# Kernel tuning notes

Hardware: AMD Instinct MI355X
Metric: run time of the kernel (lower is better)

The kernel has to match this reference:

```python
import jax, jax.numpy as jnp
import numpy as np

S_LEN, BATCH, HID, HEADS = 2048, 4, 1024, 16
HD = HID // HEADS


def setup_inputs() -> dict:
    key = jax.random.key(0)
    ks = jax.random.split(key, 6)

    def lin_w(k, out_dim, in_dim):
        return jax.random.normal(k, (out_dim, in_dim), jnp.float32) * (1.0 / np.sqrt(in_dim))

    return {
        "hidden_states": jax.random.normal(ks[0], (S_LEN, BATCH, HID), jnp.float32),
        "Wq": lin_w(ks[1], HID, HID), "bq": jnp.zeros((HID,), jnp.float32),
        "Wk": lin_w(ks[2], HID, HID), "bk": jnp.zeros((HID,), jnp.float32),
        "Wv": lin_w(ks[3], HID, HID), "bv": jnp.zeros((HID,), jnp.float32),
        "Wf": lin_w(ks[4], HEADS, HID), "bf": jnp.zeros((HEADS,), jnp.float32),
        "Wo": lin_w(ks[5], HID, HID), "bo": jnp.zeros((HID,), jnp.float32),
    }


def _forget_attention(hidden_states, Wq, bq, Wk, bk, Wv, bv, Wf, bf, Wo, bo):
    S, B, H = hidden_states.shape
    nh, hd = HEADS, HD

    def shape(x):
        return x.reshape(S, B, nh, hd)

    q = shape(hidden_states @ Wq.T + bq)
    k = shape(hidden_states @ Wk.T + bk)
    v = shape(hidden_states @ Wv.T + bv)

    # kernel_fn = elu(x) + 1
    phi_q = jax.nn.elu(q) + 1.0
    phi_k = jax.nn.elu(k) + 1.0

    f = jax.nn.sigmoid(hidden_states @ Wf.T + bf)  # [S, B, nh]

    # F_{t,j} = prod_{i=j+1}^{t} f_i  factorizes into the recurrence:
    #   S_t = f_t * S_{t-1} + phi_k_t (x) v_t ;  z_t = f_t * z_{t-1} + phi_k_t
    # out_t = (phi_q_t . S_t) / (phi_q_t . z_t + eps)
    def step(carry, xs):
        Sm, z = carry                      # [B,nh,hd,hd], [B,nh,hd]
        ft, pk, pq, vt = xs                # [B,nh], [B,nh,hd] x3
        fte = ft[..., None]
        Sm = fte[..., None] * Sm + pk[..., :, None] * vt[..., None, :]
        z = fte * z + pk
        num = jnp.einsum('bhd,bhde->bhe', pq, Sm)
        den = jnp.einsum('bhd,bhd->bh', pq, z)[..., None]
        return (Sm, z), num / (den + 1e-6)

    init = (jnp.zeros((B, nh, hd, hd), hidden_states.dtype),
            jnp.zeros((B, nh, hd), hidden_states.dtype))
    _, out = jax.lax.scan(step, init, (f, phi_k, phi_q, v))

    out = out.reshape(S, B, H) @ Wo.T + bo
    return out, f


def reference(hidden_states, Wq, bq, Wk, bk, Wv, bv, Wf, bf, Wo, bo):
    out, f = _forget_attention(hidden_states, Wq, bq, Wk, bk, Wv, bv, Wf, bf, Wo, bo)
    return (out, jnp.zeros_like(out), f)
```

## Files before the change

kernel.cpp:

```cpp
#include <hip/hip_runtime.h>
#include <hip/hip_bf16.h>
#include <math.h>

#define S_LEN 2048
#define BATCH 4
#define HID   1024
#define HEADS 16
#define HD    64
#define SB    (S_LEN*BATCH)
#define CHUNK 64
#define NCHUNK (S_LEN/CHUNK)
#define BH    (BATCH*HEADS)
#define NSTK  3200

typedef __bf16 bf16x8 __attribute__((ext_vector_type(8)));
typedef float  f32x4  __attribute__((ext_vector_type(4)));
typedef unsigned short ushort_t;
typedef unsigned short u16x8 __attribute__((ext_vector_type(8)));

__device__ __forceinline__ unsigned short f2bf(float x) {
    union { float f; unsigned int u; } un; un.f = x;
    unsigned int u = un.u;
    unsigned int r = (u + 0x7FFFu + ((u >> 16) & 1u)) >> 16;
    return (unsigned short)r;
}
__device__ __forceinline__ float bf2f(unsigned short s) {
    union { unsigned int u; float f; } un; un.u = ((unsigned int)s) << 16;
    return un.f;
}

#define NXU (SB*HID/4)
#define NW1 (NSTK*HID/4)
#define NW2 (HID*HID/4)
#define NBU (NSTK/4)
#define NTOT (NXU+NW1+NW2+NBU)

__global__ __launch_bounds__(256) void prep_kernel(
    const float* __restrict__ X,  const float* __restrict__ Wq,
    const float* __restrict__ Wk, const float* __restrict__ Wv,
    const float* __restrict__ Wf, const float* __restrict__ Wo,
    const float* __restrict__ bq, const float* __restrict__ bk,
    const float* __restrict__ bv, const float* __restrict__ bf,
    ushort_t* __restrict__ Xb, ushort_t* __restrict__ Wstk,
    ushort_t* __restrict__ Wob, float* __restrict__ bstk)
{
    const int i = blockIdx.x * 256 + threadIdx.x;
    if (i < NXU) {
        float4 v = ((const float4*)X)[i];
        ushort4 o; o.x=f2bf(v.x); o.y=f2bf(v.y); o.z=f2bf(v.z); o.w=f2bf(v.w);
        ((ushort4*)Xb)[i] = o;
    } else if (i < NXU + NW1) {
        const int idx4 = (i - NXU) * 4;
        const int row = idx4 >> 10, col = idx4 & 1023;
        float4 v;
        if      (row < 1024) v = *(const float4*)(Wq + (size_t)row*HID + col);
        else if (row < 2048) v = *(const float4*)(Wk + (size_t)(row-1024)*HID + col);
        else if (row < 3072) v = *(const float4*)(Wv + (size_t)(row-2048)*HID + col);
        else if (row < 3088) v = *(const float4*)(Wf + (size_t)(row-3072)*HID + col);
        else                 v = make_float4(0.f,0.f,0.f,0.f);
        ushort4 o; o.x=f2bf(v.x); o.y=f2bf(v.y); o.z=f2bf(v.z); o.w=f2bf(v.w);
        *(ushort4*)(Wstk + idx4) = o;
    } else if (i < NXU + NW1 + NW2) {
        const int idx4 = (i - NXU - NW1) * 4;
        float4 v = *(const float4*)(Wo + idx4);
        ushort4 o; o.x=f2bf(v.x); o.y=f2bf(v.y); o.z=f2bf(v.z); o.w=f2bf(v.w);
        *(ushort4*)(Wob + idx4) = o;
    } else if (i < NTOT) {
        const int idx4 = (i - NXU - NW1 - NW2) * 4;
        #pragma unroll
        for (int t = 0; t < 4; ++t) {
            const int c = idx4 + t;
            float v;
            if      (c < 1024) v = bq[c];
            else if (c < 2048) v = bk[c-1024];
            else if (c < 3072) v = bv[c-2048];
            else if (c < 3088) v = bf[c-3072];
            else               v = 0.f;
            bstk[c] = v;
        }
    }
}

__global__ __launch_bounds__(256) void qkvf_gemm(
    const ushort_t* __restrict__ X, const ushort_t* __restrict__ W,
    const float* __restrict__ bias,
    ushort_t* __restrict__ Q, ushort_t* __restrict__ Kr,
    ushort_t* __restrict__ KT, ushort_t* __restrict__ VT,
    float* __restrict__ f_out, float* __restrict__ logf_out)
{
    __shared__ ushort_t As[128 * 32];
    __shared__ ushort_t Bs[128 * 32];

    const int tid  = threadIdx.x;
    const int wave = tid >> 6, lane = tid & 63;
    const int waveM = wave >> 1, waveN = wave & 1;
    const int rowBase = blockIdx.y * 128;
    const int colBase = blockIdx.x * 128;
    const int K = HID;

    f32x4 acc[4][4];
    #pragma unroll
    for (int i = 0; i < 4; ++i)
        #pragma unroll
        for (int j = 0; j < 4; ++j)
            acc[i][j] = (f32x4){0.f, 0.f, 0.f, 0.f};

    const int srow = lane >> 2;
    const int scol = (lane & 3) * 8;

    const ushort_t* gA0 = X + (size_t)(rowBase + wave*16 + srow) * K + scol;
    const ushort_t* gB0 = W + (size_t)(colBase + wave*16 + srow) * K + scol;
    ushort_t* lA = As + (wave*16)*32;
    ushort_t* lB = Bs + (wave*16)*32;

    const int fr = lane & 15;
    const int fk = (lane >> 4) * 8;

    for (int k0 = 0; k0 < K; k0 += 32) {
        __builtin_amdgcn_global_load_lds(
            (const __attribute__((address_space(1))) void*)(gA0 + k0),
            (__attribute__((address_space(3))) void*)lA, 16, 0, 0);
        __builtin_amdgcn_global_load_lds(
            (const __attribute__((address_space(1))) void*)(gA0 + (size_t)64*K + k0),
            (__attribute__((address_space(3))) void*)(lA + 64*32), 16, 0, 0);
        __builtin_amdgcn_global_load_lds(
            (const __attribute__((address_space(1))) void*)(gB0 + k0),
            (__attribute__((address_space(3))) void*)lB, 16, 0, 0);
        __builtin_amdgcn_global_load_lds(
            (const __attribute__((address_space(1))) void*)(gB0 + (size_t)64*K + k0),
            (__attribute__((address_space(3))) void*)(lB + 64*32), 16, 0, 0);

        __syncthreads();

        bf16x8 a[4], b[4];
        #pragma unroll
        for (int i = 0; i < 4; ++i)
            a[i] = *(const bf16x8*)(As + (waveM*64 + i*16 + fr)*32 + fk);
        #pragma unroll
        for (int j = 0; j < 4; ++j)
            b[j] = *(const bf16x8*)(Bs + (waveN*64 + j*16 + fr)*32 + fk);

        #pragma unroll
        for (int i = 0; i < 4; ++i)
            #pragma unroll
            for (int j = 0; j < 4; ++j)
                acc[i][j] = __builtin_amdgcn_mfma_f32_16x16x32_bf16(
                    a[i], b[j], acc[i][j], 0, 0, 0);

        __syncthreads();
    }

    const int er = (lane >> 4) * 4;
    const int ec = lane & 15;
    #pragma unroll
    for (int i = 0; i < 4; ++i) {
        #pragma unroll
        for (int j = 0; j < 4; ++j) {
            const int r0 = rowBase + waveM*64 + i*16 + er;
            const int c0 = colBase + waveN*64 + j*16;
            if (c0 >= 3088) continue;
            const int c  = c0 + ec;
            const float bv = bias[c];
            #pragma unroll
            for (int k = 0; k < 4; ++k) {
                float v = acc[i][j][k] + bv;
                const int r = r0 + k;
                const int s = r >> 2, bb = r & 3;
                if (c0 < 1024) {
                    v = (v > 0.f) ? (v + 1.f) : __expf(v);
                    Q[(size_t)r * HID + c] = f2bf(v);
                } else if (c0 < 2048) {
                    v = (v > 0.f) ? (v + 1.f) : __expf(v);
                    const int cc = c - 1024;
                    const ushort_t h = f2bf(v);
                    Kr[(size_t)r * HID + cc] = h;
                    KT[(size_t)bb * ((size_t)HID*S_LEN) + (size_t)cc * S_LEN + s] = h;
                } else if (c0 < 3072) {
                    const int cc = c - 2048;
                    VT[(size_t)bb * ((size_t)HID*S_LEN) + (size_t)cc * S_LEN + s] = f2bf(v);
                } else {
                    const int n = c - 3072;
                    const float fv = 1.f / (1.f + __expf(-v));
                    f_out[(size_t)r * HEADS + n]    = fv;
                    logf_out[(size_t)r * HEADS + n] = -__logf(1.f + __expf(-v));
                }
            }
        }
    }
}

__global__ __launch_bounds__(256) void gemm_out(
    const ushort_t* __restrict__ X, const ushort_t* __restrict__ W,
    const float* __restrict__ bias, float* __restrict__ Y,
    float* __restrict__ Yzero)
{
    __shared__ ushort_t As[128 * 32];
    __shared__ ushort_t Bs[128 * 32];

    const int tid  = threadIdx.x;
    const int wave = tid >> 6, lane = tid & 63;
    const int waveM = wave >> 1, waveN = wave & 1;
    const int rowBase = blockIdx.y * 128;
    const int colBase = blockIdx.x * 128;
    const int K = HID, N = HID;

    f32x4 acc[4][4];
    #pragma unroll
    for (int i = 0; i < 4; ++i)
        #pragma unroll
        for (int j = 0; j < 4; ++j)
            acc[i][j] = (f32x4){0.f, 0.f, 0.f, 0.f};

    const int srow = lane >> 2;
    const int scol = (lane & 3) * 8;

    const ushort_t* gA0 = X + (size_t)(rowBase + wave*16 + srow) * K + scol;
    const ushort_t* gB0 = W + (size_t)(colBase + wave*16 + srow) * K + scol;
    ushort_t* lA = As + (wave*16)*32;
    ushort_t* lB = Bs + (wave*16)*32;

    const int fr = lane & 15;
    const int fk = (lane >> 4) * 8;

    for (int k0 = 0; k0 < K; k0 += 32) {
        __builtin_amdgcn_global_load_lds(
            (const __attribute__((address_space(1))) void*)(gA0 + k0),
            (__attribute__((address_space(3))) void*)lA, 16, 0, 0);
        __builtin_amdgcn_global_load_lds(
            (const __attribute__((address_space(1))) void*)(gA0 + (size_t)64*K + k0),
            (__attribute__((address_space(3))) void*)(lA + 64*32), 16, 0, 0);
        __builtin_amdgcn_global_load_lds(
            (const __attribute__((address_space(1))) void*)(gB0 + k0),
            (__attribute__((address_space(3))) void*)lB, 16, 0, 0);
        __builtin_amdgcn_global_load_lds(
            (const __attribute__((address_space(1))) void*)(gB0 + (size_t)64*K + k0),
            (__attribute__((address_space(3))) void*)(lB + 64*32), 16, 0, 0);

        __syncthreads();

        bf16x8 a[4], b[4];
        #pragma unroll
        for (int i = 0; i < 4; ++i)
            a[i] = *(const bf16x8*)(As + (waveM*64 + i*16 + fr)*32 + fk);
        #pragma unroll
        for (int j = 0; j < 4; ++j)
            b[j] = *(const bf16x8*)(Bs + (waveN*64 + j*16 + fr)*32 + fk);

        #pragma unroll
        for (int i = 0; i < 4; ++i)
            #pragma unroll
            for (int j = 0; j < 4; ++j)
                acc[i][j] = __builtin_amdgcn_mfma_f32_16x16x32_bf16(
                    a[i], b[j], acc[i][j], 0, 0, 0);

        __syncthreads();
    }

    const int er = (lane >> 4) * 4;
    const int ec = lane & 15;
    #pragma unroll
    for (int i = 0; i < 4; ++i) {
        #pragma unroll
        for (int j = 0; j < 4; ++j) {
            const int r0 = rowBase + waveM*64 + i*16 + er;
            const int c  = colBase + waveN*64 + j*16 + ec;
            const float bv = bias[c];
            #pragma unroll
            for (int k = 0; k < 4; ++k) {
                const size_t off = (size_t)(r0 + k) * N + c;
                Y[off] = acc[i][j][k] + bv;
                Yzero[off] = 0.f;
            }
        }
    }
}

__global__ __launch_bounds__(256) void pass1_kernel(
    const ushort_t* __restrict__ KTp, const ushort_t* __restrict__ VTp,
    const float* __restrict__ logf,
    float* __restrict__ Schunk, float* __restrict__ zchunk,
    float* __restrict__ Dchunk)
{
    __shared__ __align__(16) char smem[18688];
    ushort_t* vsT = (ushort_t*)smem;
    ushort_t* kTd = (ushort_t*)(smem + 9216);
    float*    exd = (float*)(smem + 18432);

    const int chunk = blockIdx.x;
    const int bh = blockIdx.y;
    const int b = bh >> 4, h = bh & 15;
    const int tid = threadIdx.x;
    const int wv = tid >> 6, ln = tid & 63;
    const int fr = ln & 15, q4 = ln >> 4;
    const size_t slot = (size_t)bh * NCHUNK + chunk;

    u16x8 vreg[2], kreg[2];
    #pragma unroll
    for (int it = 0; it < 2; ++it) {
        const int u = it*256 + tid;
        const int r = u >> 3, j8 = (u & 7) * 8;
        const size_t base = (size_t)b * ((size_t)HID*S_LEN)
                          + (size_t)(h*HD + r) * S_LEN + chunk*64 + j8;
        vreg[it] = *(const u16x8*)(VTp + base);
        kreg[it] = *(const u16x8*)(KTp + base);
    }
    if (tid < 64) {
        float v = logf[(size_t)((chunk*64 + tid)*BATCH + b) * HEADS + h];
        #pragma unroll
        for (int off = 1; off < 64; off <<= 1) {
            float n = __shfl_up(v, off);
            if (tid >= off) v += n;
        }
        const float tot = __shfl(v, 63);
        exd[tid] = __expf(tot - v);
        if (tid == 63) Dchunk[slot] = __expf(tot);
    }
    __syncthreads();

    #pragma unroll
    for (int it = 0; it < 2; ++it) {
        const int u = it*256 + tid;
        const int r = u >> 3, j8 = (u & 7) * 8;
        *(u16x8*)(vsT + r*72 + j8) = vreg[it];
        u16x8 kd;
        #pragma unroll
        for (int i = 0; i < 8; ++i) kd[i] = f2bf(bf2f(kreg[it][i]) * exd[j8+i]);
        *(u16x8*)(kTd + r*72 + j8) = kd;
    }
    __syncthreads();

    f32x4 acc[4];
    #pragma unroll
    for (int nt = 0; nt < 4; ++nt) acc[nt] = (f32x4){0.f,0.f,0.f,0.f};
    #pragma unroll
    for (int k0 = 0; k0 < 64; k0 += 32) {
        bf16x8 av = *(const bf16x8*)(vsT + (wv*16 + fr)*72 + k0 + q4*8);
        #pragma unroll
        for (int nt = 0; nt < 4; ++nt) {
            bf16x8 bk = *(const bf16x8*)(kTd + (nt*16 + fr)*72 + k0 + q4*8);
            acc[nt] = __builtin_amdgcn_mfma_f32_16x16x32_bf16(av, bk, acc[nt], 0, 0, 0);
        }
    }

    if (wv == 0) {
        u16x8 onesu;
        #pragma unroll
        for (int i = 0; i < 8; ++i) onesu[i] = 0x3F80;
        const bf16x8 ones = *(const bf16x8*)&onesu;
        f32x4 zacc[4];
        #pragma unroll
        for (int nt = 0; nt < 4; ++nt) zacc[nt] = (f32x4){0.f,0.f,0.f,0.f};
        #pragma unroll
        for (int k0 = 0; k0 < 64; k0 += 32) {
            #pragma unroll
            for (int nt = 0; nt < 4; ++nt) {
                bf16x8 bk = *(const bf16x8*)(kTd + (nt*16 + fr)*72 + k0 + q4*8);
                zacc[nt] = __builtin_amdgcn_mfma_f32_16x16x32_bf16(ones, bk, zacc[nt], 0, 0, 0);
            }
        }
        if (q4 == 0) {
            #pragma unroll
            for (int nt = 0; nt < 4; ++nt)
                zchunk[slot*64 + nt*16 + fr] = zacc[nt][0];
        }
    }

    float* sp = Schunk + slot * 4096;
    #pragma unroll
    for (int nt = 0; nt < 4; ++nt) {
        #pragma unroll
        for (int r = 0; r < 4; ++r) {
            const int e = wv*16 + q4*4 + r;
            sp[e*64 + nt*16 + fr] = acc[nt][r];
        }
    }
}

__global__ __launch_bounds__(256) void pass2_kernel(
    float* __restrict__ Schunk, float* __restrict__ zchunk,
    const float* __restrict__ Dchunk)
{
    const int bh = blockIdx.x;
    const int tid = threadIdx.x;

    float Sprev[16];
    #pragma unroll
    for (int i = 0; i < 16; ++i) Sprev[i] = 0.f;
    float zprev = 0.f;

    const size_t base  = (size_t)bh * NCHUNK * 4096;
    const size_t zbase = (size_t)bh * NCHUNK * 64;

    for (int c = 0; c < NCHUNK; ++c) {
        const float D = Dchunk[bh * NCHUNK + c];
        float* sp = Schunk + base + (size_t)c * 4096;
        float contrib[16];
        #pragma unroll
        for (int i = 0; i < 16; ++i) contrib[i] = sp[i*256 + tid];
        #pragma unroll
        for (int i = 0; i < 16; ++i) {
            sp[i*256 + tid] = Sprev[i];
            Sprev[i] = D * Sprev[i] + contrib[i];
        }
        if (tid < 64) {
            float* zp = zchunk + zbase + (size_t)c * 64;
            const float zc = zp[tid];
            zp[tid] = zprev;
            zprev = D * zprev + zc;
        }
    }
}

__global__ __launch_bounds__(256) void pass3_kernel(
    const ushort_t* __restrict__ Qp, const ushort_t* __restrict__ Kp,
    const ushort_t* __restrict__ VTp, const float* __restrict__ logf,
    const float* __restrict__ S0, const float* __restrict__ z0,
    ushort_t* __restrict__ AO)
{
    __shared__ __align__(16) char smem[28672];
    ushort_t* qs  = (ushort_t*)smem;
    ushort_t* ks  = (ushort_t*)(smem + 9216);
    ushort_t* vsT = (ushort_t*)(smem + 9216);
    ushort_t* psA = (ushort_t*)(smem + 18432);
    float* cc  = (float*)(smem + 27648);
    float* exT = (float*)(smem + 27904);
    float* qz  = (float*)(smem + 28160);
    float* den = (float*)(smem + 28416);

    const int chunk = blockIdx.x;
    const int bh = blockIdx.y;
    const int b = bh >> 4, h = bh & 15;
    const int tid = threadIdx.x;
    const int wv = tid >> 6, ln = tid & 63;
    const int fr = ln & 15, q4 = ln >> 4;
    const size_t slot = (size_t)bh * NCHUNK + chunk;

    if (tid < 64) {
        float v = logf[(size_t)((chunk*64 + tid)*BATCH + b) * HEADS + h];
        #pragma unroll
        for (int off = 1; off < 64; off <<= 1) {
            float n = __shfl_up(v, off);
            if (tid >= off) v += n;
        }
        cc[tid]  = v;
        exT[tid] = __expf(v);
    }
    #pragma unroll
    for (int it = 0; it < 2; ++it) {
        const int u = it*256 + tid;
        const int r = u >> 3, c8 = (u & 7) * 8;
        const size_t goff = (size_t)((chunk*64 + r)*BATCH + b) * HID + h*HD + c8;
        *(u16x8*)(qs + r*72 + c8) = *(const u16x8*)(Qp + goff);
        *(u16x8*)(ks + r*72 + c8) = *(const u16x8*)(Kp + goff);
    }
    __syncthreads();

    f32x4 pacc[4];
    #pragma unroll
    for (int nt = 0; nt < 4; ++nt) pacc[nt] = (f32x4){0.f,0.f,0.f,0.f};
    #pragma unroll
    for (int k0 = 0; k0 < 64; k0 += 32) {
        bf16x8 af = *(const bf16x8*)(qs + (wv*16 + fr)*72 + k0 + q4*8);
        #pragma unroll
        for (int nt = 0; nt < 4; ++nt) {
            bf16x8 bfr = *(const bf16x8*)(ks + (nt*16 + fr)*72 + k0 + q4*8);
            pacc[nt] = __builtin_amdgcn_mfma_f32_16x16x32_bf16(af, bfr, pacc[nt], 0, 0, 0);
        }
    }
    if (tid < 64) {
        float zown = z0[slot * 64 + tid];
        float s = 0.f;
        for (int d = 0; d < 64; ++d) {
            const float zd = __shfl(zown, d);
            s += bf2f(qs[tid*72 + d]) * zd;
        }
        qz[tid] = s;
    }
    __syncthreads();

    #pragma unroll
    for (int it = 0; it < 2; ++it) {
        const int u = it*256 + tid;
        const int e = u >> 3, j8 = (u & 7) * 8;
        *(u16x8*)(vsT + e*72 + j8) =
            *(const u16x8*)(VTp + (size_t)b*((size_t)HID*S_LEN)
                            + (size_t)(h*HD + e)*S_LEN + chunk*64 + j8);
    }
    {
        float rs[4] = {0.f, 0.f, 0.f, 0.f};
        float cct[4];
        #pragma unroll
        for (int r = 0; r < 4; ++r) cct[r] = cc[wv*16 + q4*4 + r];
        #pragma unroll
        for (int nt = 0; nt < 4; ++nt) {
            const int j = nt*16 + fr;
            const float ccj = cc[j];
            #pragma unroll
            for (int r = 0; r < 4; ++r) {
                const int t = wv*16 + q4*4 + r;
                float p = (j <= t) ? pacc[nt][r] * __expf(cct[r] - ccj) : 0.f;
                rs[r] += p;
                psA[t*72 + j] = f2bf(p);
            }
        }
        #pragma unroll
        for (int m = 1; m < 16; m <<= 1) {
            #pragma unroll
            for (int r = 0; r < 4; ++r) rs[r] += __shfl_xor(rs[r], m);
        }
        if (fr == 0) {
            #pragma unroll
            for (int r = 0; r < 4; ++r) {
                const int t = wv*16 + q4*4 + r;
                den[t] = rs[r] + exT[t] * qz[t] + 1e-6f;
            }
        }
    }
    __syncthreads();

    f32x4 oacc[4], oacc2[4];
    #pragma unroll
    for (int nt = 0; nt < 4; ++nt) {
        oacc[nt]  = (f32x4){0.f,0.f,0.f,0.f};
        oacc2[nt] = (f32x4){0.f,0.f,0.f,0.f};
    }
    const float* S0p = S0 + slot * 4096;
    #pragma unroll
    for (int k0 = 0; k0 < 64; k0 += 32) {
        const int k8 = k0 + q4*8;
        bf16x8 ap = *(const bf16x8*)(psA + (wv*16 + fr)*72 + k8);
        bf16x8 aq = *(const bf16x8*)(qs  + (wv*16 + fr)*72 + k8);
        #pragma unroll
        for (int nt = 0; nt < 4; ++nt) {
            bf16x8 bv = *(const bf16x8*)(vsT + (nt*16 + fr)*72 + k8);
            oacc[nt] = __builtin_amdgcn_mfma_f32_16x16x32_bf16(ap, bv, oacc[nt], 0, 0, 0);
            f32x4 s0a = *(const f32x4*)(S0p + (nt*16 + fr)*64 + k8);
            f32x4 s0b = *(const f32x4*)(S0p + (nt*16 + fr)*64 + k8 + 4);
            u16x8 sb;
            #pragma unroll
            for (int i = 0; i < 4; ++i) { sb[i] = f2bf(s0a[i]); sb[4+i] = f2bf(s0b[i]); }
            oacc2[nt] = __builtin_amdgcn_mfma_f32_16x16x32_bf16(aq, *(bf16x8*)&sb, oacc2[nt], 0, 0, 0);
        }
    }
    #pragma unroll
    for (int nt = 0; nt < 4; ++nt) {
        const int e = nt*16 + fr;
        #pragma unroll
        for (int r = 0; r < 4; ++r) {
            const int t = wv*16 + q4*4 + r;
            const float v = (oacc[nt][r] + exT[t] * oacc2[nt][r]) / den[t];
            AO[(size_t)((chunk*64 + t)*BATCH + b) * HID + h*HD + e] = f2bf(v);
        }
    }
}

extern "C" void kernel_launch(void* const* d_in, const int* in_sizes, int n_in,
                              void* d_out, int out_size, void* d_ws, size_t ws_size,
                              hipStream_t stream) {
    const float* X  = (const float*)d_in[0];
    const float* Wq = (const float*)d_in[1];
    const float* bq = (const float*)d_in[2];
    const float* Wk = (const float*)d_in[3];
    const float* bk = (const float*)d_in[4];
    const float* Wv = (const float*)d_in[5];
    const float* bv = (const float*)d_in[6];
    const float* Wf = (const float*)d_in[7];
    const float* bf = (const float*)d_in[8];
    const float* Wo = (const float*)d_in[9];
    const float* bo = (const float*)d_in[10];

    float* out = (float*)d_out;
    const size_t OUT_SLOT = (size_t)SB * HID;

    char* ws = (char*)d_ws;
    ushort_t* wsXb   = (ushort_t*)ws;
    ushort_t* wsWstk = wsXb + (size_t)SB * HID;
    ushort_t* wsWob  = wsWstk + (size_t)NSTK * HID;
    ushort_t* wsQ    = wsWob + (size_t)HID * HID;
    ushort_t* wsK    = wsQ + (size_t)SB * HID;
    ushort_t* wsKT   = wsK + (size_t)SB * HID;
    ushort_t* wsVT   = wsKT + (size_t)SB * HID;
    float* wsBstk = (float*)(wsVT + (size_t)SB * HID);
    float* wsLogf = wsBstk + NSTK;
    float* wsS    = wsLogf + (size_t)SB * HEADS;
    float* wsZ    = wsS + (size_t)BH * NCHUNK * HD * HD;
    float* wsD    = wsZ + (size_t)BH * NCHUNK * HD;

    prep_kernel<<<(NTOT + 255)/256, 256, 0, stream>>>(
        X, Wq, Wk, Wv, Wf, Wo, bq, bk, bv, bf,
        wsXb, wsWstk, wsWob, wsBstk);

    dim3 qgrid(NSTK/128, SB/128);
    qkvf_gemm<<<qgrid, 256, 0, stream>>>(
        wsXb, wsWstk, wsBstk, wsQ, wsK, wsKT, wsVT,
        out + 2*OUT_SLOT, wsLogf);

    dim3 sgrid(NCHUNK, BH);
    pass1_kernel<<<sgrid, 256, 0, stream>>>(wsKT, wsVT, wsLogf, wsS, wsZ, wsD);
    pass2_kernel<<<BH, 256, 0, stream>>>(wsS, wsZ, wsD);
    pass3_kernel<<<sgrid, 256, 0, stream>>>(wsQ, wsK, wsVT, wsLogf, wsS, wsZ, wsXb);

    dim3 ogrid(HID/128, SB/128);
    gemm_out<<<ogrid, 256, 0, stream>>>(wsXb, wsWob, bo, out, out + OUT_SLOT);
}
```

Baseline: 330.6 us.

## Drop transposed K/V global copies; transpose in shared memory and swap GEMM grid order

The QKV GEMM epilogue no longer writes the strided, uncoalesced transposed K and V buffers. It writes V in row-major layout, and pass1/pass3 transpose K and V while storing them into shared memory. This removes a scattered 2-byte global store pattern and one workspace buffer, at the cost of bank-conflicted scalar LDS writes. Both GEMMs also swap their grid axes so consecutive blocks walk along rows, which changes L2 reuse of the weight tiles.

```diff
diff --git a/kernel.cpp b/kernel.cpp
--- a/kernel.cpp
+++ b/kernel.cpp
@@ -85,7 +85,7 @@
     const ushort_t* __restrict__ X, const ushort_t* __restrict__ W,
     const float* __restrict__ bias,
     ushort_t* __restrict__ Q, ushort_t* __restrict__ Kr,
-    ushort_t* __restrict__ KT, ushort_t* __restrict__ VT,
+    ushort_t* __restrict__ V,
     float* __restrict__ f_out, float* __restrict__ logf_out)
 {
     __shared__ ushort_t As[128 * 32];
@@ -94,8 +94,8 @@
     const int tid  = threadIdx.x;
     const int wave = tid >> 6, lane = tid & 63;
     const int waveM = wave >> 1, waveN = wave & 1;
-    const int rowBase = blockIdx.y * 128;
-    const int colBase = blockIdx.x * 128;
+    const int rowBase = blockIdx.x * 128;
+    const int colBase = blockIdx.y * 128;
     const int K = HID;
 
     f32x4 acc[4][4];
@@ -165,19 +165,14 @@
             for (int k = 0; k < 4; ++k) {
                 float v = acc[i][j][k] + bv;
                 const int r = r0 + k;
-                const int s = r >> 2, bb = r & 3;
                 if (c0 < 1024) {
                     v = (v > 0.f) ? (v + 1.f) : __expf(v);
                     Q[(size_t)r * HID + c] = f2bf(v);
                 } else if (c0 < 2048) {
                     v = (v > 0.f) ? (v + 1.f) : __expf(v);
-                    const int cc = c - 1024;
-                    const ushort_t h = f2bf(v);
-                    Kr[(size_t)r * HID + cc] = h;
-                    KT[(size_t)bb * ((size_t)HID*S_LEN) + (size_t)cc * S_LEN + s] = h;
+                    Kr[(size_t)r * HID + (c - 1024)] = f2bf(v);
                 } else if (c0 < 3072) {
-                    const int cc = c - 2048;
-                    VT[(size_t)bb * ((size_t)HID*S_LEN) + (size_t)cc * S_LEN + s] = f2bf(v);
+                    V[(size_t)r * HID + (c - 2048)] = f2bf(v);
                 } else {
                     const int n = c - 3072;
                     const float fv = 1.f / (1.f + __expf(-v));
@@ -200,8 +195,8 @@
     const int tid  = threadIdx.x;
     const int wave = tid >> 6, lane = tid & 63;
     const int waveM = wave >> 1, waveN = wave & 1;
-    const int rowBase = blockIdx.y * 128;
-    const int colBase = blockIdx.x * 128;
+    const int rowBase = blockIdx.x * 128;
+    const int colBase = blockIdx.y * 128;
     const int K = HID, N = HID;
 
     f32x4 acc[4][4];
@@ -276,7 +271,7 @@
 }
 
 __global__ __launch_bounds__(256) void pass1_kernel(
-    const ushort_t* __restrict__ KTp, const ushort_t* __restrict__ VTp,
+    const ushort_t* __restrict__ Kp, const ushort_t* __restrict__ Vp,
     const float* __restrict__ logf,
     float* __restrict__ Schunk, float* __restrict__ zchunk,
     float* __restrict__ Dchunk)
@@ -298,11 +293,10 @@
     #pragma unroll
     for (int it = 0; it < 2; ++it) {
         const int u = it*256 + tid;
-        const int r = u >> 3, j8 = (u & 7) * 8;
-        const size_t base = (size_t)b * ((size_t)HID*S_LEN)
-                          + (size_t)(h*HD + r) * S_LEN + chunk*64 + j8;
-        vreg[it] = *(const u16x8*)(VTp + base);
-        kreg[it] = *(const u16x8*)(KTp + base);
+        const int j = u >> 3, d8 = (u & 7) * 8;
+        const size_t base = (size_t)((chunk*64 + j)*BATCH + b)*HID + h*HD + d8;
+        vreg[it] = *(const u16x8*)(Vp + base);
+        kreg[it] = *(const u16x8*)(Kp + base);
     }
     if (tid < 64) {
         float v = logf[(size_t)((chunk*64 + tid)*BATCH + b) * HEADS + h];
@@ -320,12 +314,13 @@
     #pragma unroll
     for (int it = 0; it < 2; ++it) {
         const int u = it*256 + tid;
-        const int r = u >> 3, j8 = (u & 7) * 8;
-        *(u16x8*)(vsT + r*72 + j8) = vreg[it];
-        u16x8 kd;
-        #pragma unroll
-        for (int i = 0; i < 8; ++i) kd[i] = f2bf(bf2f(kreg[it][i]) * exd[j8+i]);
-        *(u16x8*)(kTd + r*72 + j8) = kd;
+        const int j = u >> 3, d8 = (u & 7) * 8;
+        const float ex = exd[j];
+        #pragma unroll
+        for (int i = 0; i < 8; ++i) {
+            vsT[(d8+i)*72 + j] = vreg[it][i];
+            kTd[(d8+i)*72 + j] = f2bf(bf2f(kreg[it][i]) * ex);
+        }
     }
     __syncthreads();
 
@@ -413,7 +408,7 @@
 
 __global__ __launch_bounds__(256) void pass3_kernel(
     const ushort_t* __restrict__ Qp, const ushort_t* __restrict__ Kp,
-    const ushort_t* __restrict__ VTp, const float* __restrict__ logf,
+    const ushort_t* __restrict__ Vp, const float* __restrict__ logf,
     const float* __restrict__ S0, const float* __restrict__ z0,
     ushort_t* __restrict__ AO)
 {
@@ -435,6 +430,14 @@
     const int fr = ln & 15, q4 = ln >> 4;
     const size_t slot = (size_t)bh * NCHUNK + chunk;
 
+    u16x8 vreg[2];
+    #pragma unroll
+    for (int it = 0; it < 2; ++it) {
+        const int u = it*256 + tid;
+        const int j = u >> 3, d8 = (u & 7) * 8;
+        vreg[it] = *(const u16x8*)(Vp + (size_t)((chunk*64 + j)*BATCH + b)*HID + h*HD + d8);
+    }
+
     if (tid < 64) {
         float v = logf[(size_t)((chunk*64 + tid)*BATCH + b) * HEADS + h];
         #pragma unroll
@@ -481,10 +484,10 @@
     #pragma unroll
     for (int it = 0; it < 2; ++it) {
         const int u = it*256 + tid;
-        const int e = u >> 3, j8 = (u & 7) * 8;
-        *(u16x8*)(vsT + e*72 + j8) =
-            *(const u16x8*)(VTp + (size_t)b*((size_t)HID*S_LEN)
-                            + (size_t)(h*HD + e)*S_LEN + chunk*64 + j8);
+        const int j = u >> 3, d8 = (u & 7) * 8;
+        #pragma unroll
+        for (int i = 0; i < 8; ++i)
+            vsT[(d8+i)*72 + j] = vreg[it][i];
     }
     {
         float rs[4] = {0.f, 0.f, 0.f, 0.f};
@@ -578,9 +581,8 @@
     ushort_t* wsWob  = wsWstk + (size_t)NSTK * HID;
     ushort_t* wsQ    = wsWob + (size_t)HID * HID;
     ushort_t* wsK    = wsQ + (size_t)SB * HID;
-    ushort_t* wsKT   = wsK + (size_t)SB * HID;
-    ushort_t* wsVT   = wsKT + (size_t)SB * HID;
-    float* wsBstk = (float*)(wsVT + (size_t)SB * HID);
+    ushort_t* wsV    = wsK + (size_t)SB * HID;
+    float* wsBstk = (float*)(wsV + (size_t)SB * HID);
     float* wsLogf = wsBstk + NSTK;
     float* wsS    = wsLogf + (size_t)SB * HEADS;
     float* wsZ    = wsS + (size_t)BH * NCHUNK * HD * HD;
@@ -590,16 +592,16 @@
         X, Wq, Wk, Wv, Wf, Wo, bq, bk, bv, bf,
         wsXb, wsWstk, wsWob, wsBstk);
 
-    dim3 qgrid(NSTK/128, SB/128);
+    dim3 qgrid(SB/128, NSTK/128);
     qkvf_gemm<<<qgrid, 256, 0, stream>>>(
-        wsXb, wsWstk, wsBstk, wsQ, wsK, wsKT, wsVT,
+        wsXb, wsWstk, wsBstk, wsQ, wsK, wsV,
         out + 2*OUT_SLOT, wsLogf);
 
     dim3 sgrid(NCHUNK, BH);
-    pass1_kernel<<<sgrid, 256, 0, stream>>>(wsKT, wsVT, wsLogf, wsS, wsZ, wsD);
+    pass1_kernel<<<sgrid, 256, 0, stream>>>(wsK, wsV, wsLogf, wsS, wsZ, wsD);
     pass2_kernel<<<BH, 256, 0, stream>>>(wsS, wsZ, wsD);
-    pass3_kernel<<<sgrid, 256, 0, stream>>>(wsQ, wsK, wsVT, wsLogf, wsS, wsZ, wsXb);
-
-    dim3 ogrid(HID/128, SB/128);
+    pass3_kernel<<<sgrid, 256, 0, stream>>>(wsQ, wsK, wsV, wsLogf, wsS, wsZ, wsXb);
+
+    dim3 ogrid(SB/128, HID/128);
     gemm_out<<<ogrid, 256, 0, stream>>>(wsXb, wsWob, bo, out, out + OUT_SLOT);
 }
```

Result: faster. 300.8 us (-9.0%).
